# Optimization experiments

Hardware: AMD Instinct MI355X
Metric: run time of the kernel (lower is better)

The kernel has to match this reference:

```python
import jax, jax.numpy as jnp
import numpy as np
from jax import lax

GRID_X, GRID_Y = 8, 8
CELL = 48  # cell_pixel_size
BATCH = 64


def setup_inputs() -> dict:
    key = jax.random.key(0)
    ks = jax.random.split(key, 9)
    s = lambda *sh: 1.0 / np.sqrt(np.prod(sh[1:])) if len(sh) > 1 else 0.0
    inp = {
        "x": jax.random.normal(ks[0], (BATCH, 3, GRID_X * CELL, GRID_Y * CELL), jnp.float32),
        "conv1_w": jax.random.normal(ks[1], (16, 3, 8, 8), jnp.float32) * 0.05,
        "conv1_b": jax.random.normal(ks[2], (16,), jnp.float32) * 0.05,
        "conv2_w": jax.random.normal(ks[3], (32, 16, 4, 4), jnp.float32) * 0.05,
        "conv2_b": jax.random.normal(ks[4], (32,), jnp.float32) * 0.05,
        "fc1_w": jax.random.normal(ks[5], (256, 288), jnp.float32) * 0.05,
        "fc1_b": jax.random.normal(ks[6], (256,), jnp.float32) * 0.05,
        "fc2_w": jax.random.normal(ks[7], (4, 256), jnp.float32) * 0.05,
        "fc2_b": jax.random.normal(ks[8], (4,), jnp.float32) * 0.05,
    }
    return inp


def _conv(x, w, b, stride, pad):
    y = lax.conv_general_dilated(
        x, w, window_strides=(stride, stride),
        padding=[(pad, pad), (pad, pad)],
        dimension_numbers=("NCHW", "OIHW", "NCHW"))
    return y + b[None, :, None, None]


def reference(x, conv1_w, conv1_b, conv2_w, conv2_b, fc1_w, fc1_b, fc2_w, fc2_b):
    B = x.shape[0]
    num_cells = GRID_X * GRID_Y
    # Grid extraction: one strided reshape instead of per-cell crop loop.
    # [B,3,gx*CELL,gy*CELL] -> [B,gx,gy,3,CELL,CELL] -> [B*cells,3,CELL,CELL]
    cells = x.reshape(B, 3, GRID_X, CELL, GRID_Y, CELL)
    cells = cells.transpose(0, 2, 4, 1, 3, 5).reshape(B * num_cells, 3, CELL, CELL)
    h = jax.nn.relu(_conv(cells, conv1_w, conv1_b, stride=4, pad=2))  # [N,16,12,12]
    h = jax.nn.relu(_conv(h, conv2_w, conv2_b, stride=4, pad=1))      # [N,32,3,3]
    h = h.reshape(B * num_cells, -1)                                   # [N,288]
    h = jax.nn.relu(h @ fc1_w.T + fc1_b)
    logits = h @ fc2_w.T + fc2_b
    probs = jax.nn.softmax(logits, axis=1)
    feats = probs.reshape(B, num_cells, 4)
    return (feats[:, :, 0], feats[:, :, 1], feats[:, :, 2])
```

## Files before the change

kernel.cpp:

```cpp
#include <hip/hip_runtime.h>

typedef float f32x4 __attribute__((ext_vector_type(4)));
typedef short s16x8 __attribute__((ext_vector_type(8)));

#define CB_PLANE 2704
#define CB_ROW 52

#define WS_H2G  0
#define WS_FW1  1179648
#define WS_W1   1253376
#define WS_W2   1256448

__device__ __forceinline__ ushort f2bf(float f) {
  unsigned u = __float_as_uint(f);
  unsigned r = (u + 0x7fffu + ((u >> 16) & 1u)) >> 16;
  return (ushort)r;
}
__device__ __forceinline__ uint pk2(float a, float b) {
  return (uint)f2bf(a) | ((uint)f2bf(b) << 16);
}

__global__ void prep_kernel(const float* __restrict__ fw1,
                            const float* __restrict__ w1,
                            const float* __restrict__ w2,
                            ushort* __restrict__ ws) {
  int i = blockIdx.x * 256 + threadIdx.x;
  if (i < 73728)       ws[WS_FW1 + i] = f2bf(fw1[i]);
  else if (i < 76800)  ws[WS_W1 + i - 73728] = f2bf(w1[i - 73728]);
  else                 ws[WS_W2 + i - 76800] = f2bf(w2[i - 76800]);
}

__device__ __forceinline__ void epi1(ushort* A2, f32x4 acc, int mt, int r16,
                                     int g, float b1v) {
#pragma unroll
  for (int rr = 0; rr < 4; ++rr) {
    int m = mt * 16 + g * 4 + rr;
    int oy = m / 12, ox = m - 12 * oy;
    if (oy < 11 && ox < 11) {
      float v = fmaxf(acc[rr] + b1v, 0.f);
      int py = (oy + 1) >> 2, k2y = (oy + 1) & 3;
      int px = (ox + 1) >> 2, k2x = (ox + 1) & 3;
      A2[(py * 3 + px) * 264 + r16 * 16 + k2y * 4 + k2x] = f2bf(v);
    }
  }
}

__global__ __launch_bounds__(256, 4)
void conv_kernel(const float* __restrict__ x,
                 const ushort* __restrict__ w1b, const float* __restrict__ b1,
                 const ushort* __restrict__ w2b, const float* __restrict__ b2,
                 ushort* __restrict__ h2g)
{
  __shared__ __align__(16) ushort cb[2][3 * CB_PLANE];
  __shared__ __align__(16) ushort A2[16 * 264];

  const int t = threadIdx.x;
  const int w = t >> 6;
  const int r16 = t & 15;
  const int g = (t & 63) >> 4;
  const int cell0 = blockIdx.x * 4;

  int goff[7], eoff[7];
#pragma unroll
  for (int i = 0; i < 7; ++i) {
    int q = i * 256 + t;
    int qq = (i < 6 || t < 192) ? q : 0;
    int c = qq / 576; int r2 = qq - c * 576;
    int y = r2 / 12;  int quad = r2 - y * 12;
    goff[i] = c * 36864 + y * 96 + quad;
    eoff[i] = c * CB_PLANE + (y + 2) * CB_ROW + 2 + quad * 4;
  }
  const float4* x4 = (const float4*)x;

  float4 v[7];
  {
    int n = cell0, b = n >> 6, gg = n & 63;
    int base4 = b * 110592 + (gg >> 3) * 4608 + (gg & 7) * 12;
#pragma unroll
    for (int i = 0; i < 7; ++i)
      if (i < 6 || t < 192) v[i] = x4[base4 + goff[i]];
  }

  for (int i = t; i < 1200; i += 256) {
    int buf = i / 600, j = i - buf * 600;
    int pl = j / 200, r = j - pl * 200;
    int off;
    if (r < 52)        off = r;
    else if (r < 104)  off = 1300 + (r - 52);
    else if (r < 152)  off = (2 + (r - 104)) * 26;
    else               off = (2 + (r - 152)) * 26 + 25;
    ((uint*)cb[buf])[pl * 1352 + off] = 0u;
  }
  {
    uint4 z = make_uint4(0u, 0u, 0u, 0u);
    uint4* p2 = (uint4*)A2;
    for (int i = t; i < 528; i += 256) p2[i] = z;
  }

  s16x8 b1f[6];
#pragma unroll
  for (int s = 0; s < 6; ++s)
    b1f[s] = *(const s16x8*)&w1b[r16 * 192 + s * 32 + g * 8];
  const float b1v = b1[r16];
  const float b2v = b2[(w & 1) * 16 + r16];

#pragma unroll
  for (int i = 0; i < 7; ++i)
    if (i < 6 || t < 192) {
      uint* d = (uint*)&cb[0][eoff[i]];
      d[0] = pk2(v[i].x, v[i].y);
      d[1] = pk2(v[i].z, v[i].w);
    }

  const int mt0 = w, mt1 = w + 4;
  int m0 = mt0 * 16 + r16, m1 = mt1 * 16 + r16, m2_ = 128 + r16;
  const int rA0 = (m0 / 12) * (4 * CB_ROW) + 4 * (m0 % 12);
  const int rA1 = (m1 / 12) * (4 * CB_ROW) + 4 * (m1 % 12);
  const int rA2 = (m2_ / 12) * (4 * CB_ROW) + 4 * (m2_ % 12);

  __syncthreads();

  for (int cl = 0; cl < 4; ++cl) {
    if (cl < 3) {
      int n = cell0 + cl + 1, b = n >> 6, gg = n & 63;
      int base4 = b * 110592 + (gg >> 3) * 4608 + (gg & 7) * 12;
#pragma unroll
      for (int i = 0; i < 7; ++i)
        if (i < 6 || t < 192) v[i] = x4[base4 + goff[i]];
    }

    const ushort* cbc = cb[cl & 1];
    f32x4 a0 = (f32x4){0.f, 0.f, 0.f, 0.f};
    f32x4 a1 = (f32x4){0.f, 0.f, 0.f, 0.f};
    f32x4 a2 = (f32x4){0.f, 0.f, 0.f, 0.f};
#pragma unroll
    for (int s = 0; s < 6; ++s) {
      int sbase = (s >> 1) * CB_PLANE + ((s & 1) * 4 + g) * CB_ROW;
      s16x8 a;
      ((uint2*)&a)[0] = *(const uint2*)&cbc[sbase + rA0];
      ((uint2*)&a)[1] = *(const uint2*)&cbc[sbase + rA0 + 4];
      a0 = __builtin_amdgcn_mfma_f32_16x16x32_bf16(a, b1f[s], a0, 0, 0, 0);
      ((uint2*)&a)[0] = *(const uint2*)&cbc[sbase + rA1];
      ((uint2*)&a)[1] = *(const uint2*)&cbc[sbase + rA1 + 4];
      a1 = __builtin_amdgcn_mfma_f32_16x16x32_bf16(a, b1f[s], a1, 0, 0, 0);
      if (w == 2) {
        ((uint2*)&a)[0] = *(const uint2*)&cbc[sbase + rA2];
        ((uint2*)&a)[1] = *(const uint2*)&cbc[sbase + rA2 + 4];
        a2 = __builtin_amdgcn_mfma_f32_16x16x32_bf16(a, b1f[s], a2, 0, 0, 0);
      }
    }
    epi1(A2, a0, mt0, r16, g, b1v);
    epi1(A2, a1, mt1, r16, g, b1v);
    if (w == 2) epi1(A2, a2, 8, r16, g, b1v);

    __syncthreads();

    if (w < 2) {
      f32x4 c2acc = (f32x4){0.f, 0.f, 0.f, 0.f};
#pragma unroll
      for (int s2 = 0; s2 < 8; ++s2) {
        uint4 av = *(const uint4*)&A2[r16 * 264 + s2 * 32 + g * 8];
        s16x8 bf = *(const s16x8*)&w2b[(w * 16 + r16) * 256 + s2 * 32 + g * 8];
        c2acc = __builtin_amdgcn_mfma_f32_16x16x32_bf16(*(s16x8*)&av, bf, c2acc, 0, 0, 0);
      }
#pragma unroll
      for (int rr = 0; rr < 4; ++rr) {
        int p2 = g * 4 + rr;
        if (p2 < 9) {
          float vv = fmaxf(c2acc[rr] + b2v, 0.f);
          h2g[(cell0 + cl) * 288 + (w * 16 + r16) * 9 + p2] = f2bf(vv);
        }
      }
    }
    if (cl < 3) {
      ushort* dst = cb[(cl + 1) & 1];
#pragma unroll
      for (int i = 0; i < 7; ++i)
        if (i < 6 || t < 192) {
          uint* d = (uint*)&dst[eoff[i]];
          d[0] = pk2(v[i].x, v[i].y);
          d[1] = pk2(v[i].z, v[i].w);
        }
    }
    __syncthreads();
  }
}

__global__ __launch_bounds__(256, 4)
void fc_kernel(const ushort* __restrict__ fw1b, const float* __restrict__ fb1,
               const float* __restrict__ fw2, const float* __restrict__ fb2,
               const ushort* __restrict__ h2g, float* __restrict__ out)
{
  __shared__ __align__(16) ushort h2s[16 * 296];
  __shared__ __align__(16) float h3s[16 * 260];
  __shared__ float ls[16][4];

  const int t = threadIdx.x;
  const int w = t >> 6;
  const int r16 = t & 15;
  const int g = (t & 63) >> 4;
  const int c0 = blockIdx.x * 16;

  const uint* src = (const uint*)(h2g + c0 * 288);
  for (int j = t; j < 2304; j += 256) {
    int r = j / 144, ci = j - r * 144;
    *(uint*)&h2s[r * 296 + 2 * ci] = src[j];
  }
  __syncthreads();

  s16x8 af[9];
#pragma unroll
  for (int s = 0; s < 9; ++s)
    af[s] = *(const s16x8*)&h2s[r16 * 296 + s * 32 + g * 8];

  f32x4 fa0 = (f32x4){0.f,0.f,0.f,0.f}, fa1 = fa0, fa2 = fa0, fa3 = fa0;
#pragma unroll
  for (int s = 0; s < 9; ++s) {
    const int ko = s * 32 + g * 8;
#pragma unroll
    for (int i = 0; i < 4; ++i) {
      s16x8 bf = *(const s16x8*)&fw1b[((w * 4 + i) * 16 + r16) * 288 + ko];
      if (i == 0) fa0 = __builtin_amdgcn_mfma_f32_16x16x32_bf16(af[s], bf, fa0, 0, 0, 0);
      if (i == 1) fa1 = __builtin_amdgcn_mfma_f32_16x16x32_bf16(af[s], bf, fa1, 0, 0, 0);
      if (i == 2) fa2 = __builtin_amdgcn_mfma_f32_16x16x32_bf16(af[s], bf, fa2, 0, 0, 0);
      if (i == 3) fa3 = __builtin_amdgcn_mfma_f32_16x16x32_bf16(af[s], bf, fa3, 0, 0, 0);
    }
  }
#pragma unroll
  for (int i = 0; i < 4; ++i) {
    f32x4 fa = (i == 0) ? fa0 : (i == 1) ? fa1 : (i == 2) ? fa2 : fa3;
    int n = (w * 4 + i) * 16 + r16;
    float fb = fb1[n];
#pragma unroll
    for (int rr = 0; rr < 4; ++rr)
      h3s[(g * 4 + rr) * 260 + n] = fmaxf(fa[rr] + fb, 0.f);
  }
  __syncthreads();

  {
    int u = t >> 2, sub = t & 3;
    int cl = u >> 2, j = u & 3;
    const float4* hp = (const float4*)&h3s[cl * 260];
    const float4* wp = (const float4*)(fw2 + j * 256);
    float p = 0.f;
#pragma unroll
    for (int i = 0; i < 16; ++i) {
      int k4 = sub + 4 * i;
      float4 a = hp[k4], bb = wp[k4];
      p = fmaf(a.x, bb.x, p); p = fmaf(a.y, bb.y, p);
      p = fmaf(a.z, bb.z, p); p = fmaf(a.w, bb.w, p);
    }
    p += __shfl_xor(p, 1);
    p += __shfl_xor(p, 2);
    if (sub == 0) ls[cl][j] = p + fb2[j];
  }
  __syncthreads();

  if (t < 16) {
    float l0 = ls[t][0], l1 = ls[t][1], l2 = ls[t][2], l3 = ls[t][3];
    float m = fmaxf(fmaxf(l0, l1), fmaxf(l2, l3));
    float e0 = __expf(l0 - m), e1 = __expf(l1 - m),
          e2 = __expf(l2 - m), e3 = __expf(l3 - m);
    float inv = 1.f / (e0 + e1 + e2 + e3);
    int n = c0 + t;
    out[n] = e0 * inv;
    out[4096 + n] = e1 * inv;
    out[8192 + n] = e2 * inv;
  }
}

extern "C" void kernel_launch(void* const* d_in, const int* in_sizes, int n_in,
                              void* d_out, int out_size, void* d_ws, size_t ws_size,
                              hipStream_t stream) {
  const float* x   = (const float*)d_in[0];
  const float* w1  = (const float*)d_in[1];
  const float* b1  = (const float*)d_in[2];
  const float* w2  = (const float*)d_in[3];
  const float* b2  = (const float*)d_in[4];
  const float* fw1 = (const float*)d_in[5];
  const float* fb1 = (const float*)d_in[6];
  const float* fw2 = (const float*)d_in[7];
  const float* fb2 = (const float*)d_in[8];
  float* out = (float*)d_out;
  ushort* ws = (ushort*)d_ws;

  hipLaunchKernelGGL(prep_kernel, dim3(332), dim3(256), 0, stream,
                     fw1, w1, w2, ws);
  hipLaunchKernelGGL(conv_kernel, dim3(1024), dim3(256), 0, stream,
                     x, ws + WS_W1, b1, ws + WS_W2, b2, ws + WS_H2G);
  hipLaunchKernelGGL(fc_kernel, dim3(256), dim3(256), 0, stream,
                     ws + WS_FW1, fb1, fw2, fb2, ws + WS_H2G, out);
}
```

Before: 44.81 us.

## Single-buffer conv input staging in LDS and raise conv_kernel occupancy hint

Replaces the double-buffered LDS staging area for cell pixels with a single buffer, which roughly halves that allocation. To keep this safe, the buffer is refilled from registers only after the barrier that follows the conv1 reads. The global prefetch of the next cell is moved to the end of each iteration, so it still has a full iteration to complete. The launch bound minimum-blocks hint goes from 4 to 5, aiming for more resident blocks per CU. The tighter register budget risks spills, and with only about four blocks per CU in this grid the extra occupancy may not be used.

```diff
diff --git a/kernel.cpp b/kernel.cpp
--- a/kernel.cpp
+++ b/kernel.cpp
@@ -45,13 +45,13 @@
   }
 }
 
-__global__ __launch_bounds__(256, 4)
+__global__ __launch_bounds__(256, 5)
 void conv_kernel(const float* __restrict__ x,
                  const ushort* __restrict__ w1b, const float* __restrict__ b1,
                  const ushort* __restrict__ w2b, const float* __restrict__ b2,
                  ushort* __restrict__ h2g)
 {
-  __shared__ __align__(16) ushort cb[2][3 * CB_PLANE];
+  __shared__ __align__(16) ushort cb[3 * CB_PLANE];
   __shared__ __align__(16) ushort A2[16 * 264];
 
   const int t = threadIdx.x;
@@ -81,15 +81,14 @@
       if (i < 6 || t < 192) v[i] = x4[base4 + goff[i]];
   }
 
-  for (int i = t; i < 1200; i += 256) {
-    int buf = i / 600, j = i - buf * 600;
-    int pl = j / 200, r = j - pl * 200;
+  for (int i = t; i < 600; i += 256) {
+    int pl = i / 200, r = i - pl * 200;
     int off;
     if (r < 52)        off = r;
     else if (r < 104)  off = 1300 + (r - 52);
     else if (r < 152)  off = (2 + (r - 104)) * 26;
     else               off = (2 + (r - 152)) * 26 + 25;
-    ((uint*)cb[buf])[pl * 1352 + off] = 0u;
+    ((uint*)cb)[pl * 1352 + off] = 0u;
   }
   {
     uint4 z = make_uint4(0u, 0u, 0u, 0u);
@@ -107,10 +106,17 @@
 #pragma unroll
   for (int i = 0; i < 7; ++i)
     if (i < 6 || t < 192) {
-      uint* d = (uint*)&cb[0][eoff[i]];
+      uint* d = (uint*)&cb[eoff[i]];
       d[0] = pk2(v[i].x, v[i].y);
       d[1] = pk2(v[i].z, v[i].w);
     }
+  {
+    int n = cell0 + 1, b = n >> 6, gg = n & 63;
+    int base4 = b * 110592 + (gg >> 3) * 4608 + (gg & 7) * 12;
+#pragma unroll
+    for (int i = 0; i < 7; ++i)
+      if (i < 6 || t < 192) v[i] = x4[base4 + goff[i]];
+  }
 
   const int mt0 = w, mt1 = w + 4;
   int m0 = mt0 * 16 + r16, m1 = mt1 * 16 + r16, m2_ = 128 + r16;
@@ -121,15 +127,6 @@
   __syncthreads();
 
   for (int cl = 0; cl < 4; ++cl) {
-    if (cl < 3) {
-      int n = cell0 + cl + 1, b = n >> 6, gg = n & 63;
-      int base4 = b * 110592 + (gg >> 3) * 4608 + (gg & 7) * 12;
-#pragma unroll
-      for (int i = 0; i < 7; ++i)
-        if (i < 6 || t < 192) v[i] = x4[base4 + goff[i]];
-    }
-
-    const ushort* cbc = cb[cl & 1];
     f32x4 a0 = (f32x4){0.f, 0.f, 0.f, 0.f};
     f32x4 a1 = (f32x4){0.f, 0.f, 0.f, 0.f};
     f32x4 a2 = (f32x4){0.f, 0.f, 0.f, 0.f};
@@ -137,15 +134,15 @@
     for (int s = 0; s < 6; ++s) {
       int sbase = (s >> 1) * CB_PLANE + ((s & 1) * 4 + g) * CB_ROW;
       s16x8 a;
-      ((uint2*)&a)[0] = *(const uint2*)&cbc[sbase + rA0];
-      ((uint2*)&a)[1] = *(const uint2*)&cbc[sbase + rA0 + 4];
+      ((uint2*)&a)[0] = *(const uint2*)&cb[sbase + rA0];
+      ((uint2*)&a)[1] = *(const uint2*)&cb[sbase + rA0 + 4];
       a0 = __builtin_amdgcn_mfma_f32_16x16x32_bf16(a, b1f[s], a0, 0, 0, 0);
-      ((uint2*)&a)[0] = *(const uint2*)&cbc[sbase + rA1];
-      ((uint2*)&a)[1] = *(const uint2*)&cbc[sbase + rA1 + 4];
+      ((uint2*)&a)[0] = *(const uint2*)&cb[sbase + rA1];
+      ((uint2*)&a)[1] = *(const uint2*)&cb[sbase + rA1 + 4];
       a1 = __builtin_amdgcn_mfma_f32_16x16x32_bf16(a, b1f[s], a1, 0, 0, 0);
       if (w == 2) {
-        ((uint2*)&a)[0] = *(const uint2*)&cbc[sbase + rA2];
-        ((uint2*)&a)[1] = *(const uint2*)&cbc[sbase + rA2 + 4];
+        ((uint2*)&a)[0] = *(const uint2*)&cb[sbase + rA2];
+        ((uint2*)&a)[1] = *(const uint2*)&cb[sbase + rA2 + 4];
         a2 = __builtin_amdgcn_mfma_f32_16x16x32_bf16(a, b1f[s], a2, 0, 0, 0);
       }
     }
@@ -173,14 +170,20 @@
       }
     }
     if (cl < 3) {
-      ushort* dst = cb[(cl + 1) & 1];
 #pragma unroll
       for (int i = 0; i < 7; ++i)
         if (i < 6 || t < 192) {
-          uint* d = (uint*)&dst[eoff[i]];
+          uint* d = (uint*)&cb[eoff[i]];
           d[0] = pk2(v[i].x, v[i].y);
           d[1] = pk2(v[i].z, v[i].w);
         }
+    }
+    if (cl < 2) {
+      int n = cell0 + cl + 2, b = n >> 6, gg = n & 63;
+      int base4 = b * 110592 + (gg >> 3) * 4608 + (gg & 7) * 12;
+#pragma unroll
+      for (int i = 0; i < 7; ++i)
+        if (i < 6 || t < 192) v[i] = x4[base4 + goff[i]];
     }
     __syncthreads();
   }
```

After: 55.94 us. 1.25x slower.
